# Kernel optimization log

Measured on AMD Instinct MI355X. Metric: run time of the kernel, lower is better.

The kernel has to match this reference:

```python
import jax, jax.numpy as jnp
import numpy as np

K = 16  # buckets per block (2**treeDepth)
DEPTH = 4

_BIT_BASE = np.array([
 [-1,-1,0,-1,0,0,0,-1,0,0,0,0,0,0,0],[-1,-1,0,-1,0,0,0,1,0,0,0,0,0,0,0],
 [-1,-1,0,1,0,0,0,0,-1,0,0,0,0,0,0],[-1,-1,0,1,0,0,0,0,1,0,0,0,0,0,0],
 [-1,1,0,0,-1,0,0,0,0,-1,0,0,0,0,0],[-1,1,0,0,-1,0,0,0,0,1,0,0,0,0,0],
 [-1,1,0,0,1,0,0,0,0,0,-1,0,0,0,0],[-1,1,0,0,1,0,0,0,0,0,1,0,0,0,0],
 [1,0,-1,0,0,-1,0,0,0,0,0,-1,0,0,0],[1,0,-1,0,0,-1,0,0,0,0,0,1,0,0,0],
 [1,0,-1,0,0,1,0,0,0,0,0,0,-1,0,0],[1,0,-1,0,0,1,0,0,0,0,0,0,1,0,0],
 [1,0,1,0,0,0,-1,0,0,0,0,0,0,-1,0],[1,0,1,0,0,0,-1,0,0,0,0,0,0,1,0],
 [1,0,1,0,0,0,1,0,0,0,0,0,0,0,-1],[1,0,1,0,0,0,1,0,0,0,0,0,0,0,1]], dtype=np.float32)

def make_tree_des_matrix(C):
    # block-diagonal, but off-blocks are ONES per the original code (init with ones)
    m = np.ones((C * K, C * (K - 1)), dtype=np.float32)
    for c in range(C):
        m[c*K:(c+1)*K, c*(K-1):(c+1)*(K-1)] = _BIT_BASE
    return jnp.asarray(m)

def make_selection_matrix(C):
    base = np.zeros((K - 1, DEPTH), dtype=np.float32)
    base[0, 0] = 1.0
    for i in range(1, K - 1):
        base[i, int(np.log2(i + 1))] = 1.0
    sel = np.zeros((C * (K - 1), C * DEPTH), dtype=np.float32)
    for c in range(C):
        sel[c*(K-1):(c+1)*(K-1), c*DEPTH:(c+1)*DEPTH] = base
    return jnp.asarray(sel)

def setup_inputs() -> dict:
    key = jax.random.key(0)
    k1, k2, k3, k4 = jax.random.split(key, 4)
    N, D, C, M = 32768, 1024, 64, 1024
    inputMatrix = jax.random.normal(k1, (N, D), dtype=jnp.float32)
    dims = jax.random.randint(k2, (C * DEPTH,), 0, D)  # gather indices into input columns
    thresholds = jax.random.normal(k3, (C * (K - 1), 1), dtype=jnp.float32)
    lut = jax.random.normal(k4, (M, C, K), dtype=jnp.float32)
    return {
        "inputMatrix": inputMatrix,
        "dims": dims,
        "thresholds": thresholds,
        "lut": lut,
        "selection_matrix": make_selection_matrix(C),
        "tree_des_mat": make_tree_des_matrix(C),
    }

def reference(inputMatrix, dims, thresholds, lut, selection_matrix, tree_des_mat):
    N = inputMatrix.shape[0]
    M, C, Kb = lut.shape
    chosen = inputMatrix[:, dims]                              # [N, C*4]
    subtracted = selection_matrix @ chosen.T - thresholds      # [C*15, N]
    tanh_h = jnp.tanh(subtracted)
    sign_ste = jnp.sign(subtracted) - jax.lax.stop_gradient(tanh_h) + tanh_h
    tree = (tree_des_mat @ sign_ste).T.reshape(N, C, Kb)       # [N, C, 16]
    soft = jax.nn.softmax(tree, axis=2)
    hard = jax.nn.one_hot(jnp.argmax(soft, axis=2), Kb, dtype=soft.dtype)
    encoded = hard - jax.lax.stop_gradient(soft) + soft        # hard-forward / soft-backward STE
    # einsum('nij,kij->nki').sum(2) == full contraction over (C, K)
    out = jnp.einsum('nck,mck->nm', encoded, lut)              # [N, M]
    return out
```

## Files before the change

kernel.cpp:

```cpp
#include <hip/hip_runtime.h>
#include <stdint.h>

#define N_ROWS 32768
#define D_DIM  1024
#define C_TREES 64
#define K_LEAF 16
#define M_OUT  1024

__global__ __launch_bounds__(256) void k_transpose(const float* __restrict__ lut,
                                                   float* __restrict__ lutT) {
    __shared__ float tile[32][33];
    int bx = blockIdx.x;
    int by = blockIdx.y;
    int tx = threadIdx.x;
    int ty = threadIdx.y;
    int src_col = bx * 32 + tx;
#pragma unroll
    for (int i = 0; i < 4; ++i) {
        int src_row = by * 32 + ty + i * 8;
        tile[ty + i * 8][tx] = lut[(size_t)src_row * 1024 + src_col];
    }
    __syncthreads();
    int dst_col = by * 32 + tx;
#pragma unroll
    for (int i = 0; i < 4; ++i) {
        int dst_row = bx * 32 + ty + i * 8;
        lutT[(size_t)dst_row * 1024 + dst_col] = tile[tx][ty + i * 8];
    }
}

__global__ __launch_bounds__(256) void k_build(const float* __restrict__ lutT,
                                               float4* __restrict__ P4) {
    int j = blockIdx.x;
    int p = blockIdx.y;
    int klo = j & 15;
    int khi = j >> 4;
    int t = threadIdx.x;
    const float4* a = (const float4*)lutT + (size_t)(p * 32 + klo) * 256;
    const float4* b = (const float4*)lutT + (size_t)(p * 32 + 16 + khi) * 256;
    float4 va = a[t];
    float4 vb = b[t];
    float4 v = make_float4(va.x + vb.x, va.y + vb.y, va.z + vb.z, va.w + vb.w);
    int gsw = (t & ~7) | ((t & 7) ^ (klo & 7));
    P4[((size_t)(p * 256 + j)) * 256 + gsw] = v;
}

__global__ __launch_bounds__(256) void k_encode2(const float* __restrict__ in,
                                                 const int* __restrict__ dims,
                                                 const float* __restrict__ th,
                                                 uint8_t* __restrict__ code) {
    __shared__ float rows[8][1028];
    __shared__ float th_s[960];
    __shared__ int   dims_s[256];
    int t = threadIdx.x;
    dims_s[t] = dims[t];
    for (int i = t; i < 960; i += 256) th_s[i] = th[i];
    int n0 = blockIdx.x * 8;
    const float4* in4 = (const float4*)(in + (size_t)n0 * 1024);
#pragma unroll
    for (int i = 0; i < 8; ++i) {
        ((float4*)&rows[i][0])[t] = in4[i * 256 + t];
    }
    __syncthreads();
    int p = t >> 3;
    int r = t & 7;
    const float* trow = &rows[r][0];
    int cA = 2 * p, cB = 2 * p + 1;

    float xA[4], xB[4];
#pragma unroll
    for (int l = 0; l < 4; ++l) {
        xA[l] = trow[dims_s[cA * 4 + l]];
        xB[l] = trow[dims_s[cB * 4 + l]];
    }
    const float* tAp = &th_s[cA * 15];
    const float* tBp = &th_s[cB * 15];
    unsigned mA = 0, mB = 0;
#pragma unroll
    for (int i = 0; i < 15; ++i) {
        const int d = (i == 0) ? 0 : (i < 3) ? 1 : (i < 7) ? 2 : 3;
        mA |= ((unsigned)(xA[d] > tAp[i])) << i;
        mB |= ((unsigned)(xB[d] > tBp[i])) << i;
    }
    int nA = 0, nB = 0;
#pragma unroll
    for (int l = 0; l < 4; ++l) {
        nA = 2 * nA + 1 + ((mA >> nA) & 1);
        nB = 2 * nB + 1 + ((mB >> nB) & 1);
    }
    code[(size_t)p * N_ROWS + n0 + r] = (uint8_t)(((nB - 15) << 4) | (nA - 15));
}

__global__ __launch_bounds__(512, 4) void k_accum3(const float4* __restrict__ P4,
                                                   const uint8_t* __restrict__ code,
                                                   float* __restrict__ out) {
    __shared__ float4 sl[2][2048];

    int t  = threadIdx.x;
    int mc = t & 7;
    int ng = t >> 3;
    int m0 = blockIdx.x * 32;
    int n0 = blockIdx.y * 1024;

    auto stage = [&](int buf, int p) {
#pragma unroll
        for (int it = 0; it < 4; ++it) {
            int idx = t + it * 512;
            int row = idx >> 3;
            int ch  = idx & 7;
            const float4* src = P4 + ((size_t)(p * 256 + row)) * 256 + (m0 >> 2) + ch;
            __builtin_amdgcn_global_load_lds((const __attribute__((address_space(1))) void*)src,
                                             (__attribute__((address_space(3))) void*)(&sl[buf][idx]),
                                             16, 0, 0);
        }
    };

    float4 acc[16];
#pragma unroll
    for (int j = 0; j < 16; ++j) acc[j] = make_float4(0.f, 0.f, 0.f, 0.f);

    const uint8_t* cp = code + n0 + ng * 16;
    uint64_t cd0 = ((const uint64_t*)cp)[0];
    uint64_t cd1 = ((const uint64_t*)cp)[1];
    stage(0, 0);

    for (int p = 0; p < 32; ++p) {
        __syncthreads();
        if (p < 31) stage((p + 1) & 1, p + 1);
        uint64_t nx0 = 0, nx1 = 0;
        if (p < 31) {
            const uint64_t* np = (const uint64_t*)(cp + (size_t)(p + 1) * N_ROWS);
            nx0 = np[0]; nx1 = np[1];
        }
        int buf = p & 1;
        const float4* s = &sl[buf][0];
#pragma unroll
        for (int j = 0; j < 16; ++j) {
            int cv = (int)(((j < 8 ? cd0 : cd1) >> ((j & 7) * 8)) & 0xff);
            int idx = (cv << 3) | (mc ^ (cv & 7));
            float4 v = s[idx];
            acc[j].x += v.x; acc[j].y += v.y; acc[j].z += v.z; acc[j].w += v.w;
        }
        cd0 = nx0; cd1 = nx1;
    }

    float4* out4 = (float4*)out;
#pragma unroll
    for (int j = 0; j < 16; ++j) {
        int n = n0 + ng * 16 + j;
        out4[(size_t)n * 256 + (m0 >> 2) + mc] = acc[j];
    }
}

__global__ __launch_bounds__(256) void k_encode(const float* __restrict__ in,
                                                const int* __restrict__ dims,
                                                const float* __restrict__ th,
                                                uint8_t* __restrict__ leaf) {
    __shared__ float rows[8][1028];
    __shared__ float th_s[960];
    __shared__ int   dims_s[256];
    int t = threadIdx.x;
    dims_s[t] = dims[t];
    for (int i = t; i < 960; i += 256) th_s[i] = th[i];
    int n0 = blockIdx.x * 8;
    const float4* in4 = (const float4*)(in + (size_t)n0 * 1024);
#pragma unroll
    for (int i = 0; i < 8; ++i) {
        ((float4*)&rows[i][0])[t] = in4[i * 256 + t];
    }
    __syncthreads();
#pragma unroll
    for (int i = 0; i < 2; ++i) {
        int id = i * 256 + t;
        int c = id >> 3;
        int r = id & 7;
        int node = 0;
        const float* trow = &rows[r][0];
#pragma unroll
        for (int lvl = 0; lvl < 4; ++lvl) {
            float x   = trow[dims_s[c * 4 + lvl]];
            float thv = th_s[c * 15 + node];
            node = 2 * node + 1 + ((x > thv) ? 1 : 0);
        }
        leaf[(size_t)c * N_ROWS + n0 + r] = (uint8_t)(node - 15);
    }
}

__global__ __launch_bounds__(512) void k_accum(const float* __restrict__ lutT,
                                               const uint8_t* __restrict__ leaf,
                                               float* __restrict__ out) {
    __shared__ float4 sl[2][16][32];
    int t     = threadIdx.x;
    int mlane = t & 31;
    int ngrp  = t >> 5;
    int wave  = t >> 6;
    int lane  = t & 63;
    int srow  = 2 * wave + (lane >> 5);
    int schunk = lane & 31;
    int m0 = blockIdx.x * 128;
    int n0 = blockIdx.y * 128;
    const float4* lutT4 = (const float4*)lutT;
    auto stage = [&](int buf, int c) {
        const float4* src = lutT4 + ((size_t)(c * 16 + srow) * 256) + (m0 >> 2) + schunk;
        __builtin_amdgcn_global_load_lds((const __attribute__((address_space(1))) void*)src,
                                         (__attribute__((address_space(3))) void*)&sl[buf][2 * wave][0],
                                         16, 0, 0);
    };
    float4 acc[8];
#pragma unroll
    for (int j = 0; j < 8; ++j) acc[j] = make_float4(0.f, 0.f, 0.f, 0.f);
    const uint8_t* lp = leaf + n0 + ngrp * 8;
    uint64_t lv = *(const uint64_t*)lp;
    stage(0, 0);
#pragma unroll 2
    for (int c = 0; c < 64; ++c) {
        __syncthreads();
        if (c < 63) stage((c + 1) & 1, c + 1);
        uint64_t lv_next = (c < 63) ? *(const uint64_t*)(lp + (size_t)(c + 1) * N_ROWS) : 0ull;
        int buf = c & 1;
#pragma unroll
        for (int j = 0; j < 8; ++j) {
            int k = (int)((lv >> (8 * j)) & 15);
            float4 v = sl[buf][k][mlane];
            acc[j].x += v.x; acc[j].y += v.y; acc[j].z += v.z; acc[j].w += v.w;
        }
        lv = lv_next;
    }
    float4* out4 = (float4*)out;
#pragma unroll
    for (int j = 0; j < 8; ++j) {
        int n = n0 + ngrp * 8 + j;
        out4[(size_t)n * 256 + (m0 >> 2) + mlane] = acc[j];
    }
}

extern "C" void kernel_launch(void* const* d_in, const int* in_sizes, int n_in,
                              void* d_out, int out_size, void* d_ws, size_t ws_size,
                              hipStream_t stream) {
    const float* inputMatrix = (const float*)d_in[0];
    const int*   dims        = (const int*)d_in[1];
    const float* thresholds  = (const float*)d_in[2];
    const float* lut         = (const float*)d_in[3];
    float* out = (float*)d_out;

    float* lutT = (float*)d_ws;

    const size_t NEED = (size_t)4 * 1024 * 1024
                      + (size_t)32 * 1024 * 1024
                      + (size_t)1 * 1024 * 1024;

    if (ws_size >= NEED) {
        float4*  P4    = (float4*)((char*)d_ws + (size_t)4 * 1024 * 1024);
        uint8_t* codep = (uint8_t*)d_ws + (size_t)36 * 1024 * 1024;

        k_transpose<<<dim3(32, 32), dim3(32, 8), 0, stream>>>(lut, lutT);
        k_build<<<dim3(256, 32), 256, 0, stream>>>(lutT, P4);
        k_encode2<<<N_ROWS / 8, 256, 0, stream>>>(inputMatrix, dims, thresholds, codep);
        k_accum3<<<dim3(M_OUT / 32, N_ROWS / 1024), 512, 0, stream>>>(P4, codep, out);
    } else {
        uint8_t* leaf = (uint8_t*)d_ws + (size_t)4 * 1024 * 1024;
        k_transpose<<<dim3(32, 32), dim3(32, 8), 0, stream>>>(lut, lutT);
        k_encode<<<N_ROWS / 8, 256, 0, stream>>>(inputMatrix, dims, thresholds, leaf);
        k_accum<<<dim3(M_OUT / 128, N_ROWS / 128), 512, 0, stream>>>(lutT, leaf, out);
    }
}
```

Baseline: 337.7 us.

## Store pair-summed LUT in fp16 and widen accumulator tile per block

The precomputed pair-sum table is now stored as fp16 instead of fp32, which halves its footprint and the bytes staged into LDS per tree pair. Each 16-byte LDS read therefore carries 8 output columns, and the accumulator tiling changes to 64 columns by 512 rows per block with 8 rows per thread. The XOR bank swizzle is removed. The trade-off is fp16 rounding error in the table values, which are sums of two fp32 entries added 32 times, plus some possible LDS bank conflicts.

After: 332.3 us. No clear change (-1.6%).

```diff
diff --git a/kernel.cpp b/kernel.cpp
--- a/kernel.cpp
+++ b/kernel.cpp
@@ -6,6 +6,9 @@
 #define C_TREES 64
 #define K_LEAF 16
 #define M_OUT  1024
+
+typedef _Float16 half8v __attribute__((ext_vector_type(8)));
+typedef _Float16 half4v __attribute__((ext_vector_type(4)));
 
 __global__ __launch_bounds__(256) void k_transpose(const float* __restrict__ lut,
                                                    float* __restrict__ lutT) {
@@ -29,8 +32,8 @@
     }
 }
 
-__global__ __launch_bounds__(256) void k_build(const float* __restrict__ lutT,
-                                               float4* __restrict__ P4) {
+__global__ __launch_bounds__(256) void k_build_h(const float* __restrict__ lutT,
+                                                 _Float16* __restrict__ Ph) {
     int j = blockIdx.x;
     int p = blockIdx.y;
     int klo = j & 15;
@@ -40,9 +43,12 @@
     const float4* b = (const float4*)lutT + (size_t)(p * 32 + 16 + khi) * 256;
     float4 va = a[t];
     float4 vb = b[t];
-    float4 v = make_float4(va.x + vb.x, va.y + vb.y, va.z + vb.z, va.w + vb.w);
-    int gsw = (t & ~7) | ((t & 7) ^ (klo & 7));
-    P4[((size_t)(p * 256 + j)) * 256 + gsw] = v;
+    half4v hv;
+    hv.x = (_Float16)(va.x + vb.x);
+    hv.y = (_Float16)(va.y + vb.y);
+    hv.z = (_Float16)(va.z + vb.z);
+    hv.w = (_Float16)(va.w + vb.w);
+    ((half4v*)Ph)[(size_t)(p * 256 + j) * 256 + t] = hv;
 }
 
 __global__ __launch_bounds__(256) void k_encode2(const float* __restrict__ in,
@@ -91,7 +97,7 @@
     code[(size_t)p * N_ROWS + n0 + r] = (uint8_t)(((nB - 15) << 4) | (nA - 15));
 }
 
-__global__ __launch_bounds__(512, 4) void k_accum3(const float4* __restrict__ P4,
+__global__ __launch_bounds__(512, 4) void k_accum4(const float4* __restrict__ P4h,
                                                    const uint8_t* __restrict__ code,
                                                    float* __restrict__ out) {
     __shared__ float4 sl[2][2048];
@@ -99,8 +105,8 @@
     int t  = threadIdx.x;
     int mc = t & 7;
     int ng = t >> 3;
-    int m0 = blockIdx.x * 32;
-    int n0 = blockIdx.y * 1024;
+    int m0 = blockIdx.x * 64;
+    int n0 = blockIdx.y * 512;
 
     auto stage = [&](int buf, int p) {
 #pragma unroll
@@ -108,47 +114,47 @@
             int idx = t + it * 512;
             int row = idx >> 3;
             int ch  = idx & 7;
-            const float4* src = P4 + ((size_t)(p * 256 + row)) * 256 + (m0 >> 2) + ch;
+            const float4* src = P4h + ((size_t)(p * 256 + row)) * 128 + (m0 >> 3) + ch;
             __builtin_amdgcn_global_load_lds((const __attribute__((address_space(1))) void*)src,
                                              (__attribute__((address_space(3))) void*)(&sl[buf][idx]),
                                              16, 0, 0);
         }
     };
 
-    float4 acc[16];
-#pragma unroll
-    for (int j = 0; j < 16; ++j) acc[j] = make_float4(0.f, 0.f, 0.f, 0.f);
-
-    const uint8_t* cp = code + n0 + ng * 16;
-    uint64_t cd0 = ((const uint64_t*)cp)[0];
-    uint64_t cd1 = ((const uint64_t*)cp)[1];
+    float acc[8][8];
+#pragma unroll
+    for (int j = 0; j < 8; ++j)
+#pragma unroll
+        for (int q = 0; q < 8; ++q) acc[j][q] = 0.f;
+
+    const uint8_t* cp = code + n0 + ng * 8;
+    uint64_t cd = *(const uint64_t*)cp;
     stage(0, 0);
 
     for (int p = 0; p < 32; ++p) {
         __syncthreads();
         if (p < 31) stage((p + 1) & 1, p + 1);
-        uint64_t nx0 = 0, nx1 = 0;
-        if (p < 31) {
-            const uint64_t* np = (const uint64_t*)(cp + (size_t)(p + 1) * N_ROWS);
-            nx0 = np[0]; nx1 = np[1];
-        }
-        int buf = p & 1;
-        const float4* s = &sl[buf][0];
-#pragma unroll
-        for (int j = 0; j < 16; ++j) {
-            int cv = (int)(((j < 8 ? cd0 : cd1) >> ((j & 7) * 8)) & 0xff);
-            int idx = (cv << 3) | (mc ^ (cv & 7));
-            float4 v = s[idx];
-            acc[j].x += v.x; acc[j].y += v.y; acc[j].z += v.z; acc[j].w += v.w;
-        }
-        cd0 = nx0; cd1 = nx1;
+        uint64_t nx = 0;
+        if (p < 31) nx = *(const uint64_t*)(cp + (size_t)(p + 1) * N_ROWS);
+        const float4* s = &sl[p & 1][0];
+#pragma unroll
+        for (int j = 0; j < 8; ++j) {
+            int cv = (int)((cd >> (8 * j)) & 0xff);
+            float4 v = s[cv * 8 + mc];
+            half8v h = __builtin_bit_cast(half8v, v);
+#pragma unroll
+            for (int q = 0; q < 8; ++q) acc[j][q] += (float)h[q];
+        }
+        cd = nx;
     }
 
     float4* out4 = (float4*)out;
 #pragma unroll
-    for (int j = 0; j < 16; ++j) {
-        int n = n0 + ng * 16 + j;
-        out4[(size_t)n * 256 + (m0 >> 2) + mc] = acc[j];
+    for (int j = 0; j < 8; ++j) {
+        int n = n0 + ng * 8 + j;
+        size_t base = (size_t)n * 256 + (m0 >> 2) + mc * 2;
+        out4[base]     = make_float4(acc[j][0], acc[j][1], acc[j][2], acc[j][3]);
+        out4[base + 1] = make_float4(acc[j][4], acc[j][5], acc[j][6], acc[j][7]);
     }
 }
 
@@ -246,17 +252,17 @@
     float* lutT = (float*)d_ws;
 
     const size_t NEED = (size_t)4 * 1024 * 1024
-                      + (size_t)32 * 1024 * 1024
+                      + (size_t)16 * 1024 * 1024
                       + (size_t)1 * 1024 * 1024;
 
     if (ws_size >= NEED) {
-        float4*  P4    = (float4*)((char*)d_ws + (size_t)4 * 1024 * 1024);
-        uint8_t* codep = (uint8_t*)d_ws + (size_t)36 * 1024 * 1024;
+        _Float16* Ph   = (_Float16*)((char*)d_ws + (size_t)4 * 1024 * 1024);
+        uint8_t* codep = (uint8_t*)d_ws + (size_t)20 * 1024 * 1024;
 
         k_transpose<<<dim3(32, 32), dim3(32, 8), 0, stream>>>(lut, lutT);
-        k_build<<<dim3(256, 32), 256, 0, stream>>>(lutT, P4);
+        k_build_h<<<dim3(256, 32), 256, 0, stream>>>(lutT, Ph);
         k_encode2<<<N_ROWS / 8, 256, 0, stream>>>(inputMatrix, dims, thresholds, codep);
-        k_accum3<<<dim3(M_OUT / 32, N_ROWS / 1024), 512, 0, stream>>>(P4, codep, out);
+        k_accum4<<<dim3(M_OUT / 64, N_ROWS / 512), 512, 0, stream>>>((const float4*)Ph, codep, out);
     } else {
         uint8_t* leaf = (uint8_t*)d_ws + (size_t)4 * 1024 * 1024;
         k_transpose<<<dim3(32, 32), dim3(32, 8), 0, stream>>>(lut, lutT);
```
